# Performance work log

Hardware: AMD Instinct MI355X
Metric: run time of the kernel (lower is better)

## Reference

```python
import jax, jax.numpy as jnp
import numpy as np

B, N, D, H = 4, 256, 32, 512

def setup_inputs() -> dict:
    key = jax.random.key(0)
    ks = jax.random.split(key, 6)
    z = jax.random.normal(ks[0], (B, N, D), dtype=jnp.float32)
    motif_mask = (jax.random.uniform(ks[1], (B, N)) > 0.5).astype(jnp.float32)
    residue_mask = jnp.ones((B, N), dtype=jnp.float32)
    # Linear weights stored as (in, out); scaled like torch default init
    W1 = jax.random.normal(ks[2], (D * D, H), dtype=jnp.float32) / np.sqrt(D * D)
    b1 = jnp.zeros((H,), dtype=jnp.float32)
    W2 = jax.random.normal(ks[3], (H, H // 2), dtype=jnp.float32) / np.sqrt(H)
    b2 = jnp.zeros((H // 2,), dtype=jnp.float32)
    W3 = jax.random.normal(ks[4], (H // 2, 1), dtype=jnp.float32) / np.sqrt(H // 2)
    b3 = jnp.zeros((1,), dtype=jnp.float32)
    return {"z": z, "motif_mask": motif_mask, "residue_mask": residue_mask,
            "W1": W1, "b1": b1, "W2": W2, "b2": b2, "W3": W3, "b3": b3}

def reference(z, motif_mask, residue_mask, W1, b1, W2, b2, W3, b3):
    # kron[b,i,j, a*D+c] = z[b,i,a] * z[b,j,c]; first Linear on kron is the
    # bilinear form z_i^T W1_h z_j -- compute via two matmuls, never
    # materializing the (B,N,N,D^2) tensor.
    d = z.shape[-1]
    W1r = W1.reshape(d, d, -1)                      # (D, D, H); axis0 = z_i dim, axis1 = z_j dim
    tmp = jnp.einsum('bia,ach->bihc', z, W1r)        # (B, N, H, D)
    h1 = jax.nn.relu(jnp.einsum('bihc,bjc->bijh', tmp, z) + b1)  # (B, N, N, H)
    h2 = jax.nn.relu(jnp.einsum('bijh,hk->bijk', h1, W2) + b2)   # (B, N, N, H/2)
    contact_logits = (jnp.einsum('bijk,ko->bijo', h2, W3) + b3)[..., 0]  # (B, N, N)
    outer_mask = motif_mask[:, None, :] * motif_mask[:, :, None]
    contact_logits = contact_logits * outer_mask
    contact_map = jax.nn.sigmoid(contact_logits)
    return (contact_map, contact_logits)
```

## Files before the change

kernel.cpp:

```cpp
#include <hip/hip_runtime.h>
#include <hip/hip_bf16.h>
#include <cstdint>
#include <cstddef>

#define NB 4
#define NN 256
#define DD 32
#define HH 512

typedef __attribute__((ext_vector_type(8))) short short8;
typedef __attribute__((ext_vector_type(4))) float f32x4;
typedef __attribute__((ext_vector_type(16))) float f32x16;

static __device__ __forceinline__ unsigned cvtpk(float a, float b) {
  unsigned r;
  asm("v_cvt_pk_bf16_f32 %0, %1, %2" : "=v"(r) : "v"(a), "v"(b));
  return r;
}
static __device__ __forceinline__ unsigned short f2bf1(float a) {
  return (unsigned short)(cvtpk(a, 0.f) & 0xffffu);
}

static __device__ __forceinline__ short8 pack8(float4 a0, float4 a1) {
  union { unsigned u[4]; short8 s; } r;
  r.u[0] = cvtpk(a0.x, a0.y); r.u[1] = cvtpk(a0.z, a0.w);
  r.u[2] = cvtpk(a1.x, a1.y); r.u[3] = cvtpk(a1.z, a1.w);
  return r.s;
}

__global__ __launch_bounds__(256) void prep(const float* __restrict__ z,
                                            const float* __restrict__ W1,
                                            const float* __restrict__ W2,
                                            const float* __restrict__ motif,
                                            unsigned short* __restrict__ W2F,
                                            unsigned short* __restrict__ Tall,
                                            int* __restrict__ jlist,
                                            int* __restrict__ jcnt,
                                            int* __restrict__ wq,
                                            int* __restrict__ wqn) {
  const int blk = blockIdx.x;
  const int tid = threadIdx.x;
  if (blk < 512) {
    __shared__ unsigned short w1s[16384];
    const int nblk = blk >> 4, mgrp = blk & 15;
    const int bibase = mgrp * 64;

    #pragma unroll
    for (int r = 0; r < 16; ++r) {
      int task = r * 256 + tid;
      int row = task >> 2;
      int hq = task & 3;
      float4 v = *(const float4*)(W1 + (size_t)row * 512 + nblk * 16 + hq * 4);
      int a = row >> 5, c = row & 31;
      int quad = a >> 3, e = a & 7;
      float hv[4] = {v.x, v.y, v.z, v.w};
      #pragma unroll
      for (int vv = 0; vv < 4; ++vv) {
        int hl = hq * 4 + vv;
        int nl = hl * 32 + c;
        int w2 = nl >> 7, r7 = nl & 127;
        int l16 = r7 >> 3, nt = r7 & 7;
        w1s[((w2 * 8 + nt) * 64 + quad * 16 + l16) * 8 + e] = f2bf1(hv[vv]);
      }
    }
    __syncthreads();

    const int w2 = tid >> 6, lane = tid & 63;
    const int quad = lane >> 4, l16 = lane & 15;

    short8 bfr[8];
    #pragma unroll
    for (int nt = 0; nt < 8; ++nt)
      bfr[nt] = *(const short8*)&w1s[((w2 * 8 + nt) * 64 + lane) * 8];

    const int ncol = nblk * 512 + w2 * 128 + l16 * 8;
    #pragma unroll
    for (int mtg = 0; mtg < 2; ++mtg) {
      short8 afr[2];
      #pragma unroll
      for (int mi = 0; mi < 2; ++mi) {
        const float* zr = z + (size_t)(bibase + (mtg * 2 + mi) * 16 + l16) * 32 + quad * 8;
        float4 a0 = *(const float4*)(zr);
        float4 a1 = *(const float4*)(zr + 4);
        afr[mi] = pack8(a0, a1);
      }
      f32x4 d[2][8];
      #pragma unroll
      for (int mi = 0; mi < 2; ++mi)
        #pragma unroll
        for (int nt = 0; nt < 8; ++nt)
          d[mi][nt] = __builtin_amdgcn_mfma_f32_16x16x32_bf16(
              afr[mi], bfr[nt], (f32x4){0.f, 0.f, 0.f, 0.f}, 0, 0, 0);
      #pragma unroll
      for (int mi = 0; mi < 2; ++mi)
        #pragma unroll
        for (int r = 0; r < 4; ++r) {
          int rowbi = bibase + (mtg * 2 + mi) * 16 + quad * 4 + r;
          if (motif[rowbi] != 0.f) {
            uint4 p;
            p.x = cvtpk(d[mi][0][r], d[mi][1][r]);
            p.y = cvtpk(d[mi][2][r], d[mi][3][r]);
            p.z = cvtpk(d[mi][4][r], d[mi][5][r]);
            p.w = cvtpk(d[mi][6][r], d[mi][7][r]);
            *(uint4*)&Tall[(size_t)rowbi * 16384 + ncol] = p;
          }
        }
    }
  } else if (blk < 576) {
    int f8 = (blk - 512) * 256 + tid;
    int lane = f8 & 63;
    int nt = (f8 >> 6) & 1, s = (f8 >> 7) & 3, hc = (f8 >> 9) & 7, w = (f8 >> 12) & 3;
    int k2 = w * 64 + nt * 32 + (lane & 31);
    int hb = hc * 64 + s * 16 + (lane >> 5) * 8;
    float v[8];
    #pragma unroll
    for (int e = 0; e < 8; ++e) v[e] = W2[(hb + e) * 256 + k2];
    uint4 p;
    p.x = cvtpk(v[0], v[1]); p.y = cvtpk(v[2], v[3]);
    p.z = cvtpk(v[4], v[5]); p.w = cvtpk(v[6], v[7]);
    ((uint4*)W2F)[f8] = p;
  } else {
    __shared__ int itemc[4];
    __shared__ int baseh[4];
    const int w = tid >> 6, lane = tid & 63;
    int cnt = 0;
    if (w < NB) {
      #pragma unroll
      for (int ch = 0; ch < 4; ++ch) {
        int j = ch * 64 + lane;
        float m = motif[w * 256 + j];
        bool alive = (m != 0.f);
        unsigned long long mk = __ballot(alive);
        unsigned long long below = mk & ((1ull << lane) - 1ull);
        int pos = __popcll(below);
        if (alive) jlist[w * 256 + cnt + pos] = j;
        cnt += __popcll(mk);
      }
      if (lane == 0) {
        jcnt[w] = cnt;
        itemc[w] = cnt * ((cnt + 63) >> 6);
      }
    }
    __syncthreads();
    if (tid == 0) {
      int s = 0;
      #pragma unroll
      for (int k = 0; k < NB; ++k) { baseh[k] = s; s += itemc[k]; }
      *wqn = s;
    }
    __syncthreads();
    if (w < NB) {
      const int K = (cnt + 63) >> 6;
      const int base = baseh[w];
      int rank = 0;
      #pragma unroll
      for (int ch = 0; ch < 4; ++ch) {
        int i = ch * 64 + lane;
        bool alive = (motif[w * 256 + i] != 0.f);
        unsigned long long mk = __ballot(alive);
        unsigned long long below = mk & ((1ull << lane) - 1ull);
        int pos = __popcll(below);
        if (alive)
          for (int jt = 0; jt < K; ++jt)
            wq[base + (rank + pos) * K + jt] = (w * 256 + i) * 4 + jt;
        rank += __popcll(mk);
      }
    }
  }
}

__global__ __launch_bounds__(256) void fused(const unsigned short* __restrict__ Tall,
                                             const unsigned short* __restrict__ W2F,
                                             const float* __restrict__ z,
                                             const float* __restrict__ b1,
                                             const float* __restrict__ b2,
                                             const float* __restrict__ W3,
                                             const float* __restrict__ b3,
                                             const float* __restrict__ motif,
                                             const int* __restrict__ jlist,
                                             const int* __restrict__ jcnt,
                                             const int* __restrict__ wq,
                                             const int* __restrict__ wqn,
                                             float* __restrict__ out) {
  __shared__ unsigned short h1s[64 * 264];
  __shared__ float red[256];

  const int bx = blockIdx.x;
  const int tid = threadIdx.x;
  const size_t OUT2 = (size_t)NB * NN * NN;
  const int nq = *wqn;

  if (bx >= nq) {
    const int nf = (int)gridDim.x - nq;
    for (int p = (bx - nq) * 256 + tid; p < NB * NN * NN; p += nf * 256) {
      int bi = p >> 8, j = p & 255, b = bi >> 8;
      if (motif[bi] == 0.f || motif[b * 256 + j] == 0.f) {
        out[p] = 0.5f;
        out[OUT2 + p] = 0.f;
      }
    }
    return;
  }
  const int item = wq[bx];

  const int w = tid >> 6, lane = tid & 63;
  const int quad = lane >> 4, l16 = lane & 15;
  const int L = lane >> 5, c32 = lane & 31;

  const int bi = item >> 2, jt = item & 3;
  const int b = bi >> 8;
  const int cnt = jcnt[b];
  const int slotbase = jt * 64;
  const float mi_v = motif[bi];

  const unsigned short* Tbase = Tall + (size_t)bi * 16384 + (w * 16 + l16) * 32 + quad * 8;
  short8 tfr[8];
  #pragma unroll
  for (int q = 0; q < 8; ++q)
    tfr[q] = *(const short8*)(Tbase + q * 2048);

  short8 zfr[4];
  #pragma unroll
  for (int nt = 0; nt < 4; ++nt) {
    int slot = slotbase + nt * 16 + l16;
    int sc = slot < cnt ? slot : cnt - 1;
    int jj = jlist[b * 256 + sc] & 255;
    const float* zr = z + (size_t)(b * 256 + jj) * 32 + quad * 8;
    float4 a0 = *(const float4*)(zr);
    float4 a1 = *(const float4*)(zr + 4);
    zfr[nt] = pack8(a0, a1);
  }

  float b2v[2], w3v[2];
  #pragma unroll
  for (int nt = 0; nt < 2; ++nt) {
    int k2 = w * 64 + nt * 32 + c32;
    b2v[nt] = b2[k2];
    w3v[nt] = W3[k2];
  }

  f32x16 acc[2][2];
  #pragma unroll
  for (int mt = 0; mt < 2; ++mt)
    #pragma unroll
    for (int nt = 0; nt < 2; ++nt)
      acc[mt][nt] = (f32x16){0.f,0.f,0.f,0.f,0.f,0.f,0.f,0.f,
                             0.f,0.f,0.f,0.f,0.f,0.f,0.f,0.f};

  const unsigned short* Wp = W2F + w * 32768 + lane * 8;
  const float* b1base = b1 + w * 16 + quad * 4;

  #pragma unroll
  for (int half = 0; half < 2; ++half) {
    #pragma unroll
    for (int q = 0; q < 4; ++q) {
      float4 b1f = *(const float4*)(b1base + (half * 4 + q) * 64);
      f32x4 cin = {b1f.x, b1f.y, b1f.z, b1f.w};
      #pragma unroll
      for (int nt = 0; nt < 4; ++nt) {
        f32x4 d = __builtin_amdgcn_mfma_f32_16x16x32_bf16(
            tfr[half * 4 + q], zfr[nt], cin, 0, 0, 0);
        uint2 p;
        p.x = cvtpk(fmaxf(d[0], 0.f), fmaxf(d[1], 0.f));
        p.y = cvtpk(fmaxf(d[2], 0.f), fmaxf(d[3], 0.f));
        *(uint2*)&h1s[(nt * 16 + l16) * 264 + q * 64 + w * 16 + quad * 4] = p;
      }
    }
    __syncthreads();

    const unsigned short* Wh = Wp + half * 16384;
    const unsigned short* h1r = &h1s[c32 * 264 + L * 8];
    short8 bfp[3][2], afp[2][2];
    #pragma unroll
    for (int p = 0; p < 3; ++p) {
      bfp[p][0] = *(const short8*)(Wh + p * 1024);
      bfp[p][1] = *(const short8*)(Wh + p * 1024 + 512);
    }
    afp[0][0] = *(const short8*)(h1r);
    afp[0][1] = *(const short8*)(h1r + 32 * 264);
    afp[1][0] = *(const short8*)(h1r + 16);
    afp[1][1] = *(const short8*)(h1r + 32 * 264 + 16);
    #pragma unroll
    for (int u = 0; u < 16; ++u) {
      const int cur = u & 1, bq = u % 3;
      short8 a0 = afp[cur][0], a1 = afp[cur][1];
      short8 b0 = bfp[bq][0], b1q = bfp[bq][1];
      if (u < 14) {
        afp[cur][0] = *(const short8*)(h1r + (u + 2) * 16);
        afp[cur][1] = *(const short8*)(h1r + 32 * 264 + (u + 2) * 16);
      }
      if (u < 13) {
        bfp[bq][0] = *(const short8*)(Wh + (u + 3) * 1024);
        bfp[bq][1] = *(const short8*)(Wh + (u + 3) * 1024 + 512);
      }
      acc[0][0] = __builtin_amdgcn_mfma_f32_32x32x16_bf16(a0, b0, acc[0][0], 0, 0, 0);
      acc[0][1] = __builtin_amdgcn_mfma_f32_32x32x16_bf16(a0, b1q, acc[0][1], 0, 0, 0);
      acc[1][0] = __builtin_amdgcn_mfma_f32_32x32x16_bf16(a1, b0, acc[1][0], 0, 0, 0);
      acc[1][1] = __builtin_amdgcn_mfma_f32_32x32x16_bf16(a1, b1q, acc[1][1], 0, 0, 0);
    }
    if (half == 0) __syncthreads();
  }

  float pr[2][16];
  #pragma unroll
  for (int mt = 0; mt < 2; ++mt)
    #pragma unroll
    for (int reg = 0; reg < 16; ++reg) {
      float s = 0.f;
      #pragma unroll
      for (int nt = 0; nt < 2; ++nt) {
        float v = acc[mt][nt][reg] + b2v[nt];
        v = v > 0.f ? v : 0.f;
        s += v * w3v[nt];
      }
      s += __shfl_xor(s, 1);
      s += __shfl_xor(s, 2);
      s += __shfl_xor(s, 4);
      s += __shfl_xor(s, 8);
      s += __shfl_xor(s, 16);
      pr[mt][reg] = s;
    }
  if (c32 == 0) {
    #pragma unroll
    for (int mt = 0; mt < 2; ++mt)
      #pragma unroll
      for (int g = 0; g < 4; ++g) {
        float4 vv = {pr[mt][g * 4 + 0], pr[mt][g * 4 + 1],
                     pr[mt][g * 4 + 2], pr[mt][g * 4 + 3]};
        *(float4*)&red[w * 64 + mt * 32 + g * 8 + L * 4] = vv;
      }
  }
  __syncthreads();
  if (tid < 64) {
    int slot = slotbase + tid;
    if (slot < cnt) {
      int j = jlist[b * 256 + slot] & 255;
      float logit = red[tid] + red[64 + tid] + red[128 + tid] + red[192 + tid] + b3[0];
      float mm = mi_v * motif[b * 256 + j];
      logit *= mm;
      float map = 1.f / (1.f + expf(-logit));
      size_t idx = (size_t)bi * 256 + j;
      out[idx] = map;
      out[OUT2 + idx] = logit;
    }
  }
}

extern "C" void kernel_launch(void* const* d_in, const int* in_sizes, int n_in,
                              void* d_out, int out_size, void* d_ws, size_t ws_size,
                              hipStream_t stream) {
  const float* z     = (const float*)d_in[0];
  const float* motif = (const float*)d_in[1];
  const float* W1 = (const float*)d_in[3];
  const float* b1 = (const float*)d_in[4];
  const float* W2 = (const float*)d_in[5];
  const float* b2 = (const float*)d_in[6];
  const float* W3 = (const float*)d_in[7];
  const float* b3 = (const float*)d_in[8];
  float* out = (float*)d_out;

  char* ws = (char*)d_ws;
  unsigned short* Tall = (unsigned short*)ws;
  unsigned short* W2F  = (unsigned short*)(ws + 33554432);
  int* jlist = (int*)(ws + 33554432 + 262144);
  int* jcnt  = (int*)(ws + 33554432 + 262144 + 4096);
  int* wq    = (int*)(ws + 33554432 + 262144 + 4096 + 64);
  int* wqn   = (int*)(ws + 33554432 + 262144 + 4096 + 64 + 16384);

  prep<<<577, 256, 0, stream>>>(z, W1, W2, motif, W2F, Tall,
                                jlist, jcnt, wq, wqn);
  fused<<<4096, 256, 0, stream>>>(Tall, W2F, z, b1, b2, W3, b3, motif,
                                  jlist, jcnt, wq, wqn, out);
}
```

Baseline: 127.2 us.

## Merge prep and fused kernels into persistent megakernel with atomic work queues

Replaces the two launches (prep and fused) with one persistent kernel of 768 blocks. Blocks pull producer tasks (queue build, W2 repack, T tiles) and then consumer tasks from atomic counters. Consumers spin-wait on per-row-group and W2 readiness flags, so stage-2 work can start before all of prep finishes. This removes the launch gap and tail effect between kernels, at the cost of an added memset, spin-wait overhead, and reliance on forward progress of producer blocks.

After: 332.6 us. +161.5%, slower.

```diff
diff --git a/kernel.cpp b/kernel.cpp
--- a/kernel.cpp
+++ b/kernel.cpp
@@ -1,12 +1,11 @@
 #include <hip/hip_runtime.h>
-#include <hip/hip_bf16.h>
 #include <cstdint>
 #include <cstddef>
 
 #define NB 4
 #define NN 256
-#define DD 32
-#define HH 512
+#define NPROD 577
+#define NGRID 768
 
 typedef __attribute__((ext_vector_type(8))) short short8;
 typedef __attribute__((ext_vector_type(4))) float f32x4;
@@ -20,328 +19,356 @@
 static __device__ __forceinline__ unsigned short f2bf1(float a) {
   return (unsigned short)(cvtpk(a, 0.f) & 0xffffu);
 }
-
 static __device__ __forceinline__ short8 pack8(float4 a0, float4 a1) {
   union { unsigned u[4]; short8 s; } r;
   r.u[0] = cvtpk(a0.x, a0.y); r.u[1] = cvtpk(a0.z, a0.w);
   r.u[2] = cvtpk(a1.x, a1.y); r.u[3] = cvtpk(a1.z, a1.w);
   return r.s;
 }
-
-__global__ __launch_bounds__(256) void prep(const float* __restrict__ z,
-                                            const float* __restrict__ W1,
-                                            const float* __restrict__ W2,
-                                            const float* __restrict__ motif,
-                                            unsigned short* __restrict__ W2F,
-                                            unsigned short* __restrict__ Tall,
-                                            int* __restrict__ jlist,
-                                            int* __restrict__ jcnt,
-                                            int* __restrict__ wq,
-                                            int* __restrict__ wqn) {
-  const int blk = blockIdx.x;
-  const int tid = threadIdx.x;
-  if (blk < 512) {
-    __shared__ unsigned short w1s[16384];
-    const int nblk = blk >> 4, mgrp = blk & 15;
-    const int bibase = mgrp * 64;
-
-    #pragma unroll
-    for (int r = 0; r < 16; ++r) {
-      int task = r * 256 + tid;
-      int row = task >> 2;
-      int hq = task & 3;
-      float4 v = *(const float4*)(W1 + (size_t)row * 512 + nblk * 16 + hq * 4);
-      int a = row >> 5, c = row & 31;
-      int quad = a >> 3, e = a & 7;
-      float hv[4] = {v.x, v.y, v.z, v.w};
-      #pragma unroll
-      for (int vv = 0; vv < 4; ++vv) {
-        int hl = hq * 4 + vv;
-        int nl = hl * 32 + c;
-        int w2 = nl >> 7, r7 = nl & 127;
-        int l16 = r7 >> 3, nt = r7 & 7;
-        w1s[((w2 * 8 + nt) * 64 + quad * 16 + l16) * 8 + e] = f2bf1(hv[vv]);
-      }
-    }
-    __syncthreads();
-
-    const int w2 = tid >> 6, lane = tid & 63;
-    const int quad = lane >> 4, l16 = lane & 15;
-
-    short8 bfr[8];
-    #pragma unroll
-    for (int nt = 0; nt < 8; ++nt)
-      bfr[nt] = *(const short8*)&w1s[((w2 * 8 + nt) * 64 + lane) * 8];
-
-    const int ncol = nblk * 512 + w2 * 128 + l16 * 8;
-    #pragma unroll
-    for (int mtg = 0; mtg < 2; ++mtg) {
-      short8 afr[2];
-      #pragma unroll
-      for (int mi = 0; mi < 2; ++mi) {
-        const float* zr = z + (size_t)(bibase + (mtg * 2 + mi) * 16 + l16) * 32 + quad * 8;
-        float4 a0 = *(const float4*)(zr);
-        float4 a1 = *(const float4*)(zr + 4);
-        afr[mi] = pack8(a0, a1);
-      }
-      f32x4 d[2][8];
-      #pragma unroll
-      for (int mi = 0; mi < 2; ++mi)
-        #pragma unroll
-        for (int nt = 0; nt < 8; ++nt)
-          d[mi][nt] = __builtin_amdgcn_mfma_f32_16x16x32_bf16(
-              afr[mi], bfr[nt], (f32x4){0.f, 0.f, 0.f, 0.f}, 0, 0, 0);
-      #pragma unroll
-      for (int mi = 0; mi < 2; ++mi)
-        #pragma unroll
-        for (int r = 0; r < 4; ++r) {
-          int rowbi = bibase + (mtg * 2 + mi) * 16 + quad * 4 + r;
-          if (motif[rowbi] != 0.f) {
-            uint4 p;
-            p.x = cvtpk(d[mi][0][r], d[mi][1][r]);
-            p.y = cvtpk(d[mi][2][r], d[mi][3][r]);
-            p.z = cvtpk(d[mi][4][r], d[mi][5][r]);
-            p.w = cvtpk(d[mi][6][r], d[mi][7][r]);
-            *(uint4*)&Tall[(size_t)rowbi * 16384 + ncol] = p;
-          }
-        }
-    }
-  } else if (blk < 576) {
-    int f8 = (blk - 512) * 256 + tid;
-    int lane = f8 & 63;
-    int nt = (f8 >> 6) & 1, s = (f8 >> 7) & 3, hc = (f8 >> 9) & 7, w = (f8 >> 12) & 3;
-    int k2 = w * 64 + nt * 32 + (lane & 31);
-    int hb = hc * 64 + s * 16 + (lane >> 5) * 8;
-    float v[8];
-    #pragma unroll
-    for (int e = 0; e < 8; ++e) v[e] = W2[(hb + e) * 256 + k2];
-    uint4 p;
-    p.x = cvtpk(v[0], v[1]); p.y = cvtpk(v[2], v[3]);
-    p.z = cvtpk(v[4], v[5]); p.w = cvtpk(v[6], v[7]);
-    ((uint4*)W2F)[f8] = p;
-  } else {
-    __shared__ int itemc[4];
-    __shared__ int baseh[4];
-    const int w = tid >> 6, lane = tid & 63;
-    int cnt = 0;
-    if (w < NB) {
-      #pragma unroll
-      for (int ch = 0; ch < 4; ++ch) {
-        int j = ch * 64 + lane;
-        float m = motif[w * 256 + j];
-        bool alive = (m != 0.f);
-        unsigned long long mk = __ballot(alive);
-        unsigned long long below = mk & ((1ull << lane) - 1ull);
-        int pos = __popcll(below);
-        if (alive) jlist[w * 256 + cnt + pos] = j;
-        cnt += __popcll(mk);
-      }
-      if (lane == 0) {
-        jcnt[w] = cnt;
-        itemc[w] = cnt * ((cnt + 63) >> 6);
-      }
-    }
-    __syncthreads();
-    if (tid == 0) {
-      int s = 0;
-      #pragma unroll
-      for (int k = 0; k < NB; ++k) { baseh[k] = s; s += itemc[k]; }
-      *wqn = s;
-    }
-    __syncthreads();
-    if (w < NB) {
-      const int K = (cnt + 63) >> 6;
-      const int base = baseh[w];
-      int rank = 0;
-      #pragma unroll
-      for (int ch = 0; ch < 4; ++ch) {
-        int i = ch * 64 + lane;
-        bool alive = (motif[w * 256 + i] != 0.f);
-        unsigned long long mk = __ballot(alive);
-        unsigned long long below = mk & ((1ull << lane) - 1ull);
-        int pos = __popcll(below);
-        if (alive)
-          for (int jt = 0; jt < K; ++jt)
-            wq[base + (rank + pos) * K + jt] = (w * 256 + i) * 4 + jt;
-        rank += __popcll(mk);
-      }
-    }
-  }
-}
-
-__global__ __launch_bounds__(256) void fused(const unsigned short* __restrict__ Tall,
-                                             const unsigned short* __restrict__ W2F,
-                                             const float* __restrict__ z,
-                                             const float* __restrict__ b1,
-                                             const float* __restrict__ b2,
-                                             const float* __restrict__ W3,
-                                             const float* __restrict__ b3,
-                                             const float* __restrict__ motif,
-                                             const int* __restrict__ jlist,
-                                             const int* __restrict__ jcnt,
-                                             const int* __restrict__ wq,
-                                             const int* __restrict__ wqn,
-                                             float* __restrict__ out) {
+static __device__ __forceinline__ int aldx(int* p) {
+  return __hip_atomic_load(p, __ATOMIC_RELAXED, __HIP_MEMORY_SCOPE_AGENT);
+}
+
+__global__ __launch_bounds__(256, 3) void mega(
+    const float* __restrict__ z, const float* __restrict__ motif,
+    const float* __restrict__ W1, const float* __restrict__ b1,
+    const float* __restrict__ W2, const float* __restrict__ b2,
+    const float* __restrict__ W3, const float* __restrict__ b3,
+    unsigned short* __restrict__ W2F, unsigned short* __restrict__ Tall,
+    int* __restrict__ jlist, int* __restrict__ jcnt,
+    int* __restrict__ wq, int* __restrict__ wqn,
+    int* __restrict__ ctl, float* __restrict__ out) {
   __shared__ unsigned short h1s[64 * 264];
   __shared__ float red[256];
-
-  const int bx = blockIdx.x;
+  __shared__ int s_b;
+  __shared__ int itemc[4];
+  __shared__ int baseh[4];
+
   const int tid = threadIdx.x;
   const size_t OUT2 = (size_t)NB * NN * NN;
-  const int nq = *wqn;
-
-  if (bx >= nq) {
-    const int nf = (int)gridDim.x - nq;
-    for (int p = (bx - nq) * 256 + tid; p < NB * NN * NN; p += nf * 256) {
-      int bi = p >> 8, j = p & 255, b = bi >> 8;
-      if (motif[bi] == 0.f || motif[b * 256 + j] == 0.f) {
-        out[p] = 0.5f;
-        out[OUT2 + p] = 0.f;
-      }
-    }
-    return;
+
+  for (;;) {
+    __syncthreads();
+    if (tid == 0)
+      s_b = __hip_atomic_fetch_add(&ctl[0], 1, __ATOMIC_RELAXED, __HIP_MEMORY_SCOPE_AGENT);
+    __syncthreads();
+    const int t = s_b;
+    if (t >= NPROD) break;
+
+    if (t == 0) {
+      const int cw = tid >> 6, lane = tid & 63;
+      int cnt = 0;
+      if (cw < NB) {
+        #pragma unroll
+        for (int ch = 0; ch < 4; ++ch) {
+          int j = ch * 64 + lane;
+          float m = motif[cw * 256 + j];
+          bool alive = (m != 0.f);
+          unsigned long long mk = __ballot(alive);
+          unsigned long long below = mk & ((1ull << lane) - 1ull);
+          int pos = __popcll(below);
+          if (alive) jlist[cw * 256 + cnt + pos] = j;
+          cnt += __popcll(mk);
+        }
+        if (lane == 0) {
+          jcnt[cw] = cnt;
+          itemc[cw] = cnt * ((cnt + 63) >> 6);
+        }
+      }
+      __syncthreads();
+      if (tid == 0) {
+        int sacc = 0;
+        #pragma unroll
+        for (int k = 0; k < NB; ++k) { baseh[k] = sacc; sacc += itemc[k]; }
+        *wqn = sacc;
+      }
+      __syncthreads();
+      if (cw < NB) {
+        const int K = (cnt + 63) >> 6;
+        const int base = baseh[cw];
+        int rank = 0;
+        #pragma unroll
+        for (int ch = 0; ch < 4; ++ch) {
+          int i = ch * 64 + lane;
+          bool alive = (motif[cw * 256 + i] != 0.f);
+          unsigned long long mk = __ballot(alive);
+          unsigned long long below = mk & ((1ull << lane) - 1ull);
+          int pos = __popcll(below);
+          if (alive)
+            for (int jt2 = 0; jt2 < K; ++jt2)
+              wq[base + (rank + pos) * K + jt2] = (cw * 256 + i) * 4 + jt2;
+          rank += __popcll(mk);
+        }
+      }
+      __syncthreads();
+      if (tid == 0)
+        __hip_atomic_store(&ctl[2], 1, __ATOMIC_RELEASE, __HIP_MEMORY_SCOPE_AGENT);
+    } else if (t <= 64) {
+      int f8 = (t - 1) * 256 + tid;
+      int lane = f8 & 63;
+      int nt = (f8 >> 6) & 1, sg = (f8 >> 7) & 3, hc = (f8 >> 9) & 7, wv = (f8 >> 12) & 3;
+      int k2 = wv * 64 + nt * 32 + (lane & 31);
+      int hb = hc * 64 + sg * 16 + (lane >> 5) * 8;
+      float v[8];
+      #pragma unroll
+      for (int e = 0; e < 8; ++e) v[e] = W2[(hb + e) * 256 + k2];
+      uint4 p;
+      p.x = cvtpk(v[0], v[1]); p.y = cvtpk(v[2], v[3]);
+      p.z = cvtpk(v[4], v[5]); p.w = cvtpk(v[6], v[7]);
+      ((uint4*)W2F)[f8] = p;
+      __syncthreads();
+      if (tid == 0)
+        __hip_atomic_fetch_add(&ctl[3], 1, __ATOMIC_RELEASE, __HIP_MEMORY_SCOPE_AGENT);
+    } else {
+      const int idx = t - 65;
+      const int nblk = idx >> 4, mgrp = idx & 15;
+      const int bibase = mgrp * 64;
+      unsigned short* w1s = h1s;
+
+      #pragma unroll
+      for (int r = 0; r < 16; ++r) {
+        int task = r * 256 + tid;
+        int row = task >> 2;
+        int hq = task & 3;
+        float4 v = *(const float4*)(W1 + (size_t)row * 512 + nblk * 16 + hq * 4);
+        int a = row >> 5, c = row & 31;
+        int qd = a >> 3, e = a & 7;
+        float hv[4] = {v.x, v.y, v.z, v.w};
+        #pragma unroll
+        for (int vv = 0; vv < 4; ++vv) {
+          int hl = hq * 4 + vv;
+          int nl = hl * 32 + c;
+          int w2i = nl >> 7, r7 = nl & 127;
+          int l16i = r7 >> 3, ntc = r7 & 7;
+          w1s[((w2i * 8 + ntc) * 64 + qd * 16 + l16i) * 8 + e] = f2bf1(hv[vv]);
+        }
+      }
+      __syncthreads();
+
+      const int w2 = tid >> 6, lane = tid & 63;
+      const int qd = lane >> 4, l16 = lane & 15;
+
+      short8 bfr[8];
+      #pragma unroll
+      for (int nt = 0; nt < 8; ++nt)
+        bfr[nt] = *(const short8*)&w1s[((w2 * 8 + nt) * 64 + lane) * 8];
+
+      const int ncol = nblk * 512 + w2 * 128 + l16 * 8;
+      #pragma unroll
+      for (int mtg = 0; mtg < 2; ++mtg) {
+        short8 afr[2];
+        #pragma unroll
+        for (int mi = 0; mi < 2; ++mi) {
+          const float* zr = z + (size_t)(bibase + (mtg * 2 + mi) * 16 + l16) * 32 + qd * 8;
+          float4 a0 = *(const float4*)(zr);
+          float4 a1 = *(const float4*)(zr + 4);
+          afr[mi] = pack8(a0, a1);
+        }
+        f32x4 d[2][8];
+        #pragma unroll
+        for (int mi = 0; mi < 2; ++mi)
+          #pragma unroll
+          for (int nt = 0; nt < 8; ++nt)
+            d[mi][nt] = __builtin_amdgcn_mfma_f32_16x16x32_bf16(
+                afr[mi], bfr[nt], (f32x4){0.f, 0.f, 0.f, 0.f}, 0, 0, 0);
+        #pragma unroll
+        for (int mi = 0; mi < 2; ++mi)
+          #pragma unroll
+          for (int r = 0; r < 4; ++r) {
+            int rowbi = bibase + (mtg * 2 + mi) * 16 + qd * 4 + r;
+            if (motif[rowbi] != 0.f) {
+              uint4 p;
+              p.x = cvtpk(d[mi][0][r], d[mi][1][r]);
+              p.y = cvtpk(d[mi][2][r], d[mi][3][r]);
+              p.z = cvtpk(d[mi][4][r], d[mi][5][r]);
+              p.w = cvtpk(d[mi][6][r], d[mi][7][r]);
+              *(uint4*)&Tall[(size_t)rowbi * 16384 + ncol] = p;
+            }
+          }
+      }
+      __syncthreads();
+      if (tid == 0)
+        __hip_atomic_fetch_add(&ctl[4 + mgrp], 1, __ATOMIC_RELEASE, __HIP_MEMORY_SCOPE_AGENT);
+    }
   }
-  const int item = wq[bx];
-
-  const int w = tid >> 6, lane = tid & 63;
-  const int quad = lane >> 4, l16 = lane & 15;
-  const int L = lane >> 5, c32 = lane & 31;
-
-  const int bi = item >> 2, jt = item & 3;
-  const int b = bi >> 8;
-  const int cnt = jcnt[b];
-  const int slotbase = jt * 64;
-  const float mi_v = motif[bi];
-
-  const unsigned short* Tbase = Tall + (size_t)bi * 16384 + (w * 16 + l16) * 32 + quad * 8;
-  short8 tfr[8];
-  #pragma unroll
-  for (int q = 0; q < 8; ++q)
-    tfr[q] = *(const short8*)(Tbase + q * 2048);
-
-  short8 zfr[4];
-  #pragma unroll
-  for (int nt = 0; nt < 4; ++nt) {
-    int slot = slotbase + nt * 16 + l16;
-    int sc = slot < cnt ? slot : cnt - 1;
-    int jj = jlist[b * 256 + sc] & 255;
-    const float* zr = z + (size_t)(b * 256 + jj) * 32 + quad * 8;
-    float4 a0 = *(const float4*)(zr);
-    float4 a1 = *(const float4*)(zr + 4);
-    zfr[nt] = pack8(a0, a1);
-  }
-
-  float b2v[2], w3v[2];
-  #pragma unroll
-  for (int nt = 0; nt < 2; ++nt) {
-    int k2 = w * 64 + nt * 32 + c32;
-    b2v[nt] = b2[k2];
-    w3v[nt] = W3[k2];
-  }
-
-  f32x16 acc[2][2];
-  #pragma unroll
-  for (int mt = 0; mt < 2; ++mt)
-    #pragma unroll
-    for (int nt = 0; nt < 2; ++nt)
-      acc[mt][nt] = (f32x16){0.f,0.f,0.f,0.f,0.f,0.f,0.f,0.f,
-                             0.f,0.f,0.f,0.f,0.f,0.f,0.f,0.f};
-
-  const unsigned short* Wp = W2F + w * 32768 + lane * 8;
-  const float* b1base = b1 + w * 16 + quad * 4;
-
-  #pragma unroll
-  for (int half = 0; half < 2; ++half) {
-    #pragma unroll
-    for (int q = 0; q < 4; ++q) {
-      float4 b1f = *(const float4*)(b1base + (half * 4 + q) * 64);
-      f32x4 cin = {b1f.x, b1f.y, b1f.z, b1f.w};
-      #pragma unroll
-      for (int nt = 0; nt < 4; ++nt) {
-        f32x4 d = __builtin_amdgcn_mfma_f32_16x16x32_bf16(
-            tfr[half * 4 + q], zfr[nt], cin, 0, 0, 0);
-        uint2 p;
-        p.x = cvtpk(fmaxf(d[0], 0.f), fmaxf(d[1], 0.f));
-        p.y = cvtpk(fmaxf(d[2], 0.f), fmaxf(d[3], 0.f));
-        *(uint2*)&h1s[(nt * 16 + l16) * 264 + q * 64 + w * 16 + quad * 4] = p;
-      }
-    }
-    __syncthreads();
-
-    const unsigned short* Wh = Wp + half * 16384;
-    const unsigned short* h1r = &h1s[c32 * 264 + L * 8];
-    short8 bfp[3][2], afp[2][2];
-    #pragma unroll
-    for (int p = 0; p < 3; ++p) {
-      bfp[p][0] = *(const short8*)(Wh + p * 1024);
-      bfp[p][1] = *(const short8*)(Wh + p * 1024 + 512);
-    }
-    afp[0][0] = *(const short8*)(h1r);
-    afp[0][1] = *(const short8*)(h1r + 32 * 264);
-    afp[1][0] = *(const short8*)(h1r + 16);
-    afp[1][1] = *(const short8*)(h1r + 32 * 264 + 16);
-    #pragma unroll
-    for (int u = 0; u < 16; ++u) {
-      const int cur = u & 1, bq = u % 3;
-      short8 a0 = afp[cur][0], a1 = afp[cur][1];
-      short8 b0 = bfp[bq][0], b1q = bfp[bq][1];
-      if (u < 14) {
-        afp[cur][0] = *(const short8*)(h1r + (u + 2) * 16);
-        afp[cur][1] = *(const short8*)(h1r + 32 * 264 + (u + 2) * 16);
-      }
-      if (u < 13) {
-        bfp[bq][0] = *(const short8*)(Wh + (u + 3) * 1024);
-        bfp[bq][1] = *(const short8*)(Wh + (u + 3) * 1024 + 512);
-      }
-      acc[0][0] = __builtin_amdgcn_mfma_f32_32x32x16_bf16(a0, b0, acc[0][0], 0, 0, 0);
-      acc[0][1] = __builtin_amdgcn_mfma_f32_32x32x16_bf16(a0, b1q, acc[0][1], 0, 0, 0);
-      acc[1][0] = __builtin_amdgcn_mfma_f32_32x32x16_bf16(a1, b0, acc[1][0], 0, 0, 0);
-      acc[1][1] = __builtin_amdgcn_mfma_f32_32x32x16_bf16(a1, b1q, acc[1][1], 0, 0, 0);
-    }
-    if (half == 0) __syncthreads();
-  }
-
-  float pr[2][16];
-  #pragma unroll
-  for (int mt = 0; mt < 2; ++mt)
-    #pragma unroll
-    for (int reg = 0; reg < 16; ++reg) {
-      float s = 0.f;
-      #pragma unroll
-      for (int nt = 0; nt < 2; ++nt) {
-        float v = acc[mt][nt][reg] + b2v[nt];
-        v = v > 0.f ? v : 0.f;
-        s += v * w3v[nt];
-      }
-      s += __shfl_xor(s, 1);
-      s += __shfl_xor(s, 2);
-      s += __shfl_xor(s, 4);
-      s += __shfl_xor(s, 8);
-      s += __shfl_xor(s, 16);
-      pr[mt][reg] = s;
-    }
-  if (c32 == 0) {
-    #pragma unroll
-    for (int mt = 0; mt < 2; ++mt)
-      #pragma unroll
-      for (int g = 0; g < 4; ++g) {
-        float4 vv = {pr[mt][g * 4 + 0], pr[mt][g * 4 + 1],
-                     pr[mt][g * 4 + 2], pr[mt][g * 4 + 3]};
-        *(float4*)&red[w * 64 + mt * 32 + g * 8 + L * 4] = vv;
-      }
+
+  if (tid == 0) {
+    while (aldx(&ctl[2]) == 0) __builtin_amdgcn_s_sleep(1);
+    asm volatile("" ::: "memory");
+    s_b = *wqn;
   }
   __syncthreads();
-  if (tid < 64) {
-    int slot = slotbase + tid;
-    if (slot < cnt) {
-      int j = jlist[b * 256 + slot] & 255;
-      float logit = red[tid] + red[64 + tid] + red[128 + tid] + red[192 + tid] + b3[0];
-      float mm = mi_v * motif[b * 256 + j];
-      logit *= mm;
-      float map = 1.f / (1.f + expf(-logit));
-      size_t idx = (size_t)bi * 256 + j;
-      out[idx] = map;
-      out[OUT2 + idx] = logit;
+  const int nq = s_b;
+
+  for (;;) {
+    __syncthreads();
+    if (tid == 0)
+      s_b = __hip_atomic_fetch_add(&ctl[1], 1, __ATOMIC_RELAXED, __HIP_MEMORY_SCOPE_AGENT);
+    __syncthreads();
+    const int t = s_b;
+    if (t >= nq + 64) break;
+
+    if (t >= nq) {
+      const int c = t - nq;
+      for (int p = c * 4096 + tid; p < (c + 1) * 4096; p += 256) {
+        int bi = p >> 8, j = p & 255, b = bi >> 8;
+        if (motif[bi] == 0.f || motif[b * 256 + j] == 0.f) {
+          out[p] = 0.5f;
+          out[OUT2 + p] = 0.f;
+        }
+      }
+      continue;
+    }
+
+    const int item = wq[t];
+    const int w = tid >> 6, lane = tid & 63;
+    const int quad = lane >> 4, l16 = lane & 15;
+    const int L = lane >> 5, c32 = lane & 31;
+
+    const int bi = item >> 2, jt = item & 3;
+    const int b = bi >> 8;
+    const int cnt = jcnt[b];
+    const int slotbase = jt * 64;
+    const float mi_v = motif[bi];
+
+    short8 zfr[4];
+    #pragma unroll
+    for (int nt = 0; nt < 4; ++nt) {
+      int slot = slotbase + nt * 16 + l16;
+      int sc = slot < cnt ? slot : cnt - 1;
+      int jj = jlist[b * 256 + sc] & 255;
+      const float* zr = z + (size_t)(b * 256 + jj) * 32 + quad * 8;
+      float4 a0 = *(const float4*)(zr);
+      float4 a1 = *(const float4*)(zr + 4);
+      zfr[nt] = pack8(a0, a1);
+    }
+
+    float b2v[2], w3v[2];
+    #pragma unroll
+    for (int nt = 0; nt < 2; ++nt) {
+      int k2 = w * 64 + nt * 32 + c32;
+      b2v[nt] = b2[k2];
+      w3v[nt] = W3[k2];
+    }
+
+    if (tid == 0) {
+      const int g = bi >> 6;
+      while (aldx(&ctl[4 + g]) < 32) __builtin_amdgcn_s_sleep(1);
+      while (aldx(&ctl[3]) < 64) __builtin_amdgcn_s_sleep(1);
+    }
+    __syncthreads();
+    asm volatile("" ::: "memory");
+
+    const unsigned short* Tbase = Tall + (size_t)bi * 16384 + (w * 16 + l16) * 32 + quad * 8;
+    short8 tfr[8];
+    #pragma unroll
+    for (int q = 0; q < 8; ++q)
+      tfr[q] = *(const short8*)(Tbase + q * 2048);
+
+    f32x16 acc[2][2];
+    #pragma unroll
+    for (int mt = 0; mt < 2; ++mt)
+      #pragma unroll
+      for (int nt = 0; nt < 2; ++nt)
+        acc[mt][nt] = (f32x16){0.f,0.f,0.f,0.f,0.f,0.f,0.f,0.f,
+                               0.f,0.f,0.f,0.f,0.f,0.f,0.f,0.f};
+
+    const unsigned short* Wp = W2F + w * 32768 + lane * 8;
+    const float* b1base = b1 + w * 16 + quad * 4;
+
+    #pragma unroll
+    for (int half = 0; half < 2; ++half) {
+      #pragma unroll
+      for (int q = 0; q < 4; ++q) {
+        float4 b1f = *(const float4*)(b1base + (half * 4 + q) * 64);
+        f32x4 cin = {b1f.x, b1f.y, b1f.z, b1f.w};
+        #pragma unroll
+        for (int nt = 0; nt < 4; ++nt) {
+          f32x4 d = __builtin_amdgcn_mfma_f32_16x16x32_bf16(
+              tfr[half * 4 + q], zfr[nt], cin, 0, 0, 0);
+          uint2 p;
+          p.x = cvtpk(fmaxf(d[0], 0.f), fmaxf(d[1], 0.f));
+          p.y = cvtpk(fmaxf(d[2], 0.f), fmaxf(d[3], 0.f));
+          *(uint2*)&h1s[(nt * 16 + l16) * 264 + q * 64 + w * 16 + quad * 4] = p;
+        }
+      }
+      __syncthreads();
+
+      const unsigned short* Wh = Wp + half * 16384;
+      const unsigned short* h1r = &h1s[c32 * 264 + L * 8];
+      short8 bfp[3][2], afp[2][2];
+      #pragma unroll
+      for (int p = 0; p < 3; ++p) {
+        bfp[p][0] = *(const short8*)(Wh + p * 1024);
+        bfp[p][1] = *(const short8*)(Wh + p * 1024 + 512);
+      }
+      afp[0][0] = *(const short8*)(h1r);
+      afp[0][1] = *(const short8*)(h1r + 32 * 264);
+      afp[1][0] = *(const short8*)(h1r + 16);
+      afp[1][1] = *(const short8*)(h1r + 32 * 264 + 16);
+      #pragma unroll
+      for (int u = 0; u < 16; ++u) {
+        const int cur = u & 1, bq = u % 3;
+        short8 a0 = afp[cur][0], a1 = afp[cur][1];
+        short8 b0 = bfp[bq][0], b1q = bfp[bq][1];
+        if (u < 14) {
+          afp[cur][0] = *(const short8*)(h1r + (u + 2) * 16);
+          afp[cur][1] = *(const short8*)(h1r + 32 * 264 + (u + 2) * 16);
+        }
+        if (u < 13) {
+          bfp[bq][0] = *(const short8*)(Wh + (u + 3) * 1024);
+          bfp[bq][1] = *(const short8*)(Wh + (u + 3) * 1024 + 512);
+        }
+        acc[0][0] = __builtin_amdgcn_mfma_f32_32x32x16_bf16(a0, b0, acc[0][0], 0, 0, 0);
+        acc[0][1] = __builtin_amdgcn_mfma_f32_32x32x16_bf16(a0, b1q, acc[0][1], 0, 0, 0);
+        acc[1][0] = __builtin_amdgcn_mfma_f32_32x32x16_bf16(a1, b0, acc[1][0], 0, 0, 0);
+        acc[1][1] = __builtin_amdgcn_mfma_f32_32x32x16_bf16(a1, b1q, acc[1][1], 0, 0, 0);
+      }
+      if (half == 0) __syncthreads();
+    }
+
+    float pr[2][16];
+    #pragma unroll
+    for (int mt = 0; mt < 2; ++mt)
+      #pragma unroll
+      for (int reg = 0; reg < 16; ++reg) {
+        float s = 0.f;
+        #pragma unroll
+        for (int nt = 0; nt < 2; ++nt) {
+          float v = acc[mt][nt][reg] + b2v[nt];
+          v = v > 0.f ? v : 0.f;
+          s += v * w3v[nt];
+        }
+        s += __shfl_xor(s, 1);
+        s += __shfl_xor(s, 2);
+        s += __shfl_xor(s, 4);
+        s += __shfl_xor(s, 8);
+        s += __shfl_xor(s, 16);
+        pr[mt][reg] = s;
+      }
+    if (c32 == 0) {
+      #pragma unroll
+      for (int mt = 0; mt < 2; ++mt)
+        #pragma unroll
+        for (int g = 0; g < 4; ++g) {
+          float4 vv = {pr[mt][g * 4 + 0], pr[mt][g * 4 + 1],
+                       pr[mt][g * 4 + 2], pr[mt][g * 4 + 3]};
+          *(float4*)&red[w * 64 + mt * 32 + g * 8 + L * 4] = vv;
+        }
+    }
+    __syncthreads();
+    if (tid < 64) {
+      int slot = slotbase + tid;
+      if (slot < cnt) {
+        int j = jlist[b * 256 + slot] & 255;
+        float logit = red[tid] + red[64 + tid] + red[128 + tid] + red[192 + tid] + b3[0];
+        float mm = mi_v * motif[b * 256 + j];
+        logit *= mm;
+        float map = 1.f / (1.f + expf(-logit));
+        size_t idx = (size_t)bi * 256 + j;
+        out[idx] = map;
+        out[OUT2 + idx] = logit;
+      }
     }
   }
 }
@@ -366,9 +393,9 @@
   int* jcnt  = (int*)(ws + 33554432 + 262144 + 4096);
   int* wq    = (int*)(ws + 33554432 + 262144 + 4096 + 64);
   int* wqn   = (int*)(ws + 33554432 + 262144 + 4096 + 64 + 16384);
-
-  prep<<<577, 256, 0, stream>>>(z, W1, W2, motif, W2F, Tall,
-                                jlist, jcnt, wq, wqn);
-  fused<<<4096, 256, 0, stream>>>(Tall, W2F, z, b1, b2, W3, b3, motif,
-                                  jlist, jcnt, wq, wqn, out);
-}
+  int* ctl   = (int*)(ws + 33554432 + 262144 + 4096 + 64 + 16384 + 256);
+
+  hipMemsetAsync(ctl, 0, 128, stream);
+  mega<<<NGRID, 256, 0, stream>>>(z, motif, W1, b1, W2, b2, W3, b3,
+                                  W2F, Tall, jlist, jcnt, wq, wqn, ctl, out);
+}
```

## Double j-tile per block to 128 with 512-thread blocks sharing W2 fragments

Applied to the files above, without the earlier changes.

Each work item now covers 128 j columns instead of 64, using 8 waves per block. Waves 0-3 and 4-7 each compute h1 for one 64-column half into a doubled LDS tile. In the second GEMM each wave owns 32 output channels across all 128 rows, so every W2 fragment load feeds four MFMAs. This halves the number of work items and the repeated T and W2 loads per output, in exchange for more LDS, more accumulator registers, an 8-way final reduction and lower occupancy. The grid is cut from 4096 to 2304 blocks.

After: 150.1 us. 18.0% more time.

```diff
diff --git a/kernel.cpp b/kernel.cpp
--- a/kernel.cpp
+++ b/kernel.cpp
@@ -137,8 +137,9 @@
         cnt += __popcll(mk);
       }
       if (lane == 0) {
+        int K = (cnt + 63) >> 6;
         jcnt[w] = cnt;
-        itemc[w] = cnt * ((cnt + 63) >> 6);
+        itemc[w] = cnt * ((K + 1) >> 1);
       }
     }
     __syncthreads();
@@ -151,6 +152,7 @@
     __syncthreads();
     if (w < NB) {
       const int K = (cnt + 63) >> 6;
+      const int KP = (K + 1) >> 1;
       const int base = baseh[w];
       int rank = 0;
       #pragma unroll
@@ -161,15 +163,15 @@
         unsigned long long below = mk & ((1ull << lane) - 1ull);
         int pos = __popcll(below);
         if (alive)
-          for (int jt = 0; jt < K; ++jt)
-            wq[base + (rank + pos) * K + jt] = (w * 256 + i) * 4 + jt;
+          for (int jp = 0; jp < KP; ++jp)
+            wq[base + (rank + pos) * KP + jp] = (w * 256 + i) * 4 + jp * 2;
         rank += __popcll(mk);
       }
     }
   }
 }
 
-__global__ __launch_bounds__(256) void fused(const unsigned short* __restrict__ Tall,
+__global__ __launch_bounds__(512) void fused(const unsigned short* __restrict__ Tall,
                                              const unsigned short* __restrict__ W2F,
                                              const float* __restrict__ z,
                                              const float* __restrict__ b1,
@@ -182,8 +184,8 @@
                                              const int* __restrict__ wq,
                                              const int* __restrict__ wqn,
                                              float* __restrict__ out) {
-  __shared__ unsigned short h1s[64 * 264];
-  __shared__ float red[256];
+  __shared__ unsigned short h1s[128 * 264];
+  __shared__ float red[1024];
 
   const int bx = blockIdx.x;
   const int tid = threadIdx.x;
@@ -192,7 +194,7 @@
 
   if (bx >= nq) {
     const int nf = (int)gridDim.x - nq;
-    for (int p = (bx - nq) * 256 + tid; p < NB * NN * NN; p += nf * 256) {
+    for (int p = (bx - nq) * 512 + tid; p < NB * NN * NN; p += nf * 512) {
       int bi = p >> 8, j = p & 255, b = bi >> 8;
       if (motif[bi] == 0.f || motif[b * 256 + j] == 0.f) {
         out[p] = 0.5f;
@@ -206,14 +208,16 @@
   const int w = tid >> 6, lane = tid & 63;
   const int quad = lane >> 4, l16 = lane & 15;
   const int L = lane >> 5, c32 = lane & 31;
-
-  const int bi = item >> 2, jt = item & 3;
+  const int wv3 = w & 3;
+  const int hg = (w >> 2) * 64;
+
+  const int bi = item >> 2, jp = (item & 3) >> 1;
   const int b = bi >> 8;
   const int cnt = jcnt[b];
-  const int slotbase = jt * 64;
+  const int slotbase = jp * 128;
   const float mi_v = motif[bi];
 
-  const unsigned short* Tbase = Tall + (size_t)bi * 16384 + (w * 16 + l16) * 32 + quad * 8;
+  const unsigned short* Tbase = Tall + (size_t)bi * 16384 + (wv3 * 16 + l16) * 32 + quad * 8;
   short8 tfr[8];
   #pragma unroll
   for (int q = 0; q < 8; ++q)
@@ -222,7 +226,7 @@
   short8 zfr[4];
   #pragma unroll
   for (int nt = 0; nt < 4; ++nt) {
-    int slot = slotbase + nt * 16 + l16;
+    int slot = slotbase + hg + nt * 16 + l16;
     int sc = slot < cnt ? slot : cnt - 1;
     int jj = jlist[b * 256 + sc] & 255;
     const float* zr = z + (size_t)(b * 256 + jj) * 32 + quad * 8;
@@ -231,24 +235,18 @@
     zfr[nt] = pack8(a0, a1);
   }
 
-  float b2v[2], w3v[2];
-  #pragma unroll
-  for (int nt = 0; nt < 2; ++nt) {
-    int k2 = w * 64 + nt * 32 + c32;
-    b2v[nt] = b2[k2];
-    w3v[nt] = W3[k2];
-  }
-
-  f32x16 acc[2][2];
-  #pragma unroll
-  for (int mt = 0; mt < 2; ++mt)
-    #pragma unroll
-    for (int nt = 0; nt < 2; ++nt)
-      acc[mt][nt] = (f32x16){0.f,0.f,0.f,0.f,0.f,0.f,0.f,0.f,
-                             0.f,0.f,0.f,0.f,0.f,0.f,0.f,0.f};
-
-  const unsigned short* Wp = W2F + w * 32768 + lane * 8;
-  const float* b1base = b1 + w * 16 + quad * 4;
+  const int k2 = w * 32 + c32;
+  const float b2s = b2[k2];
+  const float w3s = W3[k2];
+
+  f32x16 acc[4];
+  #pragma unroll
+  for (int mt = 0; mt < 4; ++mt)
+    acc[mt] = (f32x16){0.f,0.f,0.f,0.f,0.f,0.f,0.f,0.f,
+                       0.f,0.f,0.f,0.f,0.f,0.f,0.f,0.f};
+
+  const unsigned short* Wp = W2F + (w >> 1) * 32768 + (w & 1) * 512 + lane * 8;
+  const float* b1base = b1 + wv3 * 16 + quad * 4;
 
   #pragma unroll
   for (int half = 0; half < 2; ++half) {
@@ -263,56 +261,51 @@
         uint2 p;
         p.x = cvtpk(fmaxf(d[0], 0.f), fmaxf(d[1], 0.f));
         p.y = cvtpk(fmaxf(d[2], 0.f), fmaxf(d[3], 0.f));
-        *(uint2*)&h1s[(nt * 16 + l16) * 264 + q * 64 + w * 16 + quad * 4] = p;
+        *(uint2*)&h1s[(hg + nt * 16 + l16) * 264 + q * 64 + wv3 * 16 + quad * 4] = p;
       }
     }
     __syncthreads();
 
     const unsigned short* Wh = Wp + half * 16384;
     const unsigned short* h1r = &h1s[c32 * 264 + L * 8];
-    short8 bfp[3][2], afp[2][2];
-    #pragma unroll
-    for (int p = 0; p < 3; ++p) {
-      bfp[p][0] = *(const short8*)(Wh + p * 1024);
-      bfp[p][1] = *(const short8*)(Wh + p * 1024 + 512);
-    }
-    afp[0][0] = *(const short8*)(h1r);
-    afp[0][1] = *(const short8*)(h1r + 32 * 264);
-    afp[1][0] = *(const short8*)(h1r + 16);
-    afp[1][1] = *(const short8*)(h1r + 32 * 264 + 16);
+    short8 bfp[3], afp[4][2];
+    #pragma unroll
+    for (int p = 0; p < 3; ++p)
+      bfp[p] = *(const short8*)(Wh + p * 1024);
+    #pragma unroll
+    for (int mt = 0; mt < 4; ++mt) {
+      afp[mt][0] = *(const short8*)(h1r + mt * 32 * 264);
+      afp[mt][1] = *(const short8*)(h1r + mt * 32 * 264 + 16);
+    }
     #pragma unroll
     for (int u = 0; u < 16; ++u) {
       const int cur = u & 1, bq = u % 3;
-      short8 a0 = afp[cur][0], a1 = afp[cur][1];
-      short8 b0 = bfp[bq][0], b1q = bfp[bq][1];
+      short8 a0 = afp[0][cur], a1 = afp[1][cur], a2 = afp[2][cur], a3 = afp[3][cur];
+      short8 bf = bfp[bq];
       if (u < 14) {
-        afp[cur][0] = *(const short8*)(h1r + (u + 2) * 16);
-        afp[cur][1] = *(const short8*)(h1r + 32 * 264 + (u + 2) * 16);
-      }
-      if (u < 13) {
-        bfp[bq][0] = *(const short8*)(Wh + (u + 3) * 1024);
-        bfp[bq][1] = *(const short8*)(Wh + (u + 3) * 1024 + 512);
-      }
-      acc[0][0] = __builtin_amdgcn_mfma_f32_32x32x16_bf16(a0, b0, acc[0][0], 0, 0, 0);
-      acc[0][1] = __builtin_amdgcn_mfma_f32_32x32x16_bf16(a0, b1q, acc[0][1], 0, 0, 0);
-      acc[1][0] = __builtin_amdgcn_mfma_f32_32x32x16_bf16(a1, b0, acc[1][0], 0, 0, 0);
-      acc[1][1] = __builtin_amdgcn_mfma_f32_32x32x16_bf16(a1, b1q, acc[1][1], 0, 0, 0);
+        afp[0][cur] = *(const short8*)(h1r + (u + 2) * 16);
+        afp[1][cur] = *(const short8*)(h1r + 32 * 264 + (u + 2) * 16);
+        afp[2][cur] = *(const short8*)(h1r + 64 * 264 + (u + 2) * 16);
+        afp[3][cur] = *(const short8*)(h1r + 96 * 264 + (u + 2) * 16);
+      }
+      if (u < 13)
+        bfp[bq] = *(const short8*)(Wh + (u + 3) * 1024);
+      acc[0] = __builtin_amdgcn_mfma_f32_32x32x16_bf16(a0, bf, acc[0], 0, 0, 0);
+      acc[1] = __builtin_amdgcn_mfma_f32_32x32x16_bf16(a1, bf, acc[1], 0, 0, 0);
+      acc[2] = __builtin_amdgcn_mfma_f32_32x32x16_bf16(a2, bf, acc[2], 0, 0, 0);
+      acc[3] = __builtin_amdgcn_mfma_f32_32x32x16_bf16(a3, bf, acc[3], 0, 0, 0);
     }
     if (half == 0) __syncthreads();
   }
 
-  float pr[2][16];
-  #pragma unroll
-  for (int mt = 0; mt < 2; ++mt)
+  float pr[4][16];
+  #pragma unroll
+  for (int mt = 0; mt < 4; ++mt)
     #pragma unroll
     for (int reg = 0; reg < 16; ++reg) {
-      float s = 0.f;
-      #pragma unroll
-      for (int nt = 0; nt < 2; ++nt) {
-        float v = acc[mt][nt][reg] + b2v[nt];
-        v = v > 0.f ? v : 0.f;
-        s += v * w3v[nt];
-      }
+      float v = acc[mt][reg] + b2s;
+      v = v > 0.f ? v : 0.f;
+      float s = v * w3s;
       s += __shfl_xor(s, 1);
       s += __shfl_xor(s, 2);
       s += __shfl_xor(s, 4);
@@ -322,20 +315,22 @@
     }
   if (c32 == 0) {
     #pragma unroll
-    for (int mt = 0; mt < 2; ++mt)
+    for (int mt = 0; mt < 4; ++mt)
       #pragma unroll
       for (int g = 0; g < 4; ++g) {
         float4 vv = {pr[mt][g * 4 + 0], pr[mt][g * 4 + 1],
                      pr[mt][g * 4 + 2], pr[mt][g * 4 + 3]};
-        *(float4*)&red[w * 64 + mt * 32 + g * 8 + L * 4] = vv;
+        *(float4*)&red[w * 128 + mt * 32 + g * 8 + L * 4] = vv;
       }
   }
   __syncthreads();
-  if (tid < 64) {
+  if (tid < 128) {
     int slot = slotbase + tid;
     if (slot < cnt) {
       int j = jlist[b * 256 + slot] & 255;
-      float logit = red[tid] + red[64 + tid] + red[128 + tid] + red[192 + tid] + b3[0];
+      float logit = b3[0];
+      #pragma unroll
+      for (int wv = 0; wv < 8; ++wv) logit += red[wv * 128 + tid];
       float mm = mi_v * motif[b * 256 + j];
       logit *= mm;
       float map = 1.f / (1.f + expf(-logit));
@@ -369,6 +364,6 @@
 
   prep<<<577, 256, 0, stream>>>(z, W1, W2, motif, W2F, Tall,
                                 jlist, jcnt, wq, wqn);
-  fused<<<4096, 256, 0, stream>>>(Tall, W2F, z, b1, b2, W3, b3, motif,
+  fused<<<2304, 512, 0, stream>>>(Tall, W2F, z, b1, b2, W3, b3, motif,
                                   jlist, jcnt, wq, wqn, out);
 }
```
